# Performance work log

Measured on AMD Instinct MI355X. Metric: run time of the kernel, lower is better.

The kernel has to match this reference:

```python
import jax, jax.numpy as jnp
import numpy as np

LOG_2PI = 1.8378770664093453  # log(2*pi)

B, N_FEAT = 4096, 1024
R, K, D = 64, 32, 16  # n_regions, n_batch (distributions per region), region size


def setup_inputs() -> dict:
    key = jax.random.key(0)
    k1, k2, k3, k4 = jax.random.split(key, 4)
    x = jax.random.normal(k1, (B, N_FEAT), dtype=jnp.float32)
    # Regions: partition-like index sets over the feature space (equal size D).
    regions = jax.random.randint(k2, (R, D), 0, N_FEAT, dtype=jnp.int64)
    # Per-region diag-Gaussian params (means ~ N(0, 0.1), scales near 1.0).
    means = 0.1 * jax.random.normal(k3, (R, K, D), dtype=jnp.float32)
    scales = 0.9 + 0.2 * jax.random.uniform(k4, (R, K, D), dtype=jnp.float32)
    return {"x": x, "regions": regions, "means": means, "scales": scales}


def reference(x, regions, means, scales):
    # Gather per-region features in one shot: [B, R, D]
    xg = x[:, regions]
    # Diag-Gaussian log-prob, broadcast over the K distributions per region.
    # z: [B, R, K, D]
    z = (xg[:, :, None, :] - means[None]) / scales[None]
    log_det = jnp.sum(jnp.log(scales), axis=-1)  # [R, K]
    ll = -0.5 * jnp.sum(z * z, axis=-1) - log_det[None] - 0.5 * D * LOG_2PI
    return ll  # [B, R, K] == stack over regions of MVNDiag.log_prob
```

## Files before the change

kernel.cpp:

```cpp
#include <hip/hip_runtime.h>

#define NB 4096
#define NF 1024
#define NR 64
#define NK 32
#define ND 16
#define BT 8
#define RT 32
#define HALF_D_LOG2PI 14.702988531274762f

__global__ __launch_bounds__(256) void prep_kernel(
    const float* __restrict__ means, const float* __restrict__ scales,
    float* __restrict__ isv, float* __restrict__ nmv, float* __restrict__ cv)
{
    int p = blockIdx.x * 256 + threadIdx.x;
    if (p >= NR * NK) return;
    const float4* m4 = (const float4*)(means + p * ND);
    const float4* s4 = (const float4*)(scales + p * ND);
    float4* i4 = (float4*)(isv + p * ND);
    float4* n4 = (float4*)(nmv + p * ND);
    float ld = 0.f;
#pragma unroll
    for (int q = 0; q < 4; ++q) {
        float4 m = m4[q], s = s4[q];
        float4 iv, nv;
        iv.x = 1.f / s.x; iv.y = 1.f / s.y; iv.z = 1.f / s.z; iv.w = 1.f / s.w;
        nv.x = -m.x * iv.x; nv.y = -m.y * iv.y; nv.z = -m.z * iv.z; nv.w = -m.w * iv.w;
        ld += logf(s.x) + logf(s.y) + logf(s.z) + logf(s.w);
        i4[q] = iv; n4[q] = nv;
    }
    cv[p] = -ld - HALF_D_LOG2PI;
}

__global__ __launch_bounds__(256) void GaussianLayer_64003602645438_kernel(
    const float* __restrict__ x,
    const int* __restrict__ regions,
    const float* __restrict__ isv,
    const float* __restrict__ nmv,
    const float* __restrict__ cv,
    float* __restrict__ out)
{
    __shared__ float xs[BT][NF];
    __shared__ float xg[BT][RT][ND];
    __shared__ int   ridx[RT * ND];

    const int t  = threadIdx.x;
    const int b0 = blockIdx.x * BT;
    const int r0 = blockIdx.y * RT;

    for (int j = t; j < RT * ND; j += 256)
        ridx[j] = regions[r0 * ND + j];

    {
        const float4* xsrc = (const float4*)(x + (size_t)b0 * NF);
        float4* xdst = (float4*)(&xs[0][0]);
#pragma unroll
        for (int j = t; j < BT * NF / 4; j += 256)
            xdst[j] = xsrc[j];
    }
    __syncthreads();

    for (int j = t; j < BT * RT * ND; j += 256) {
        int d  = j & (ND - 1);
        int rl = (j >> 4) & (RT - 1);
        int b  = j >> 9;
        xg[b][rl][d] = xs[b][ridx[rl * ND + d]];
    }
    __syncthreads();

    const int k   = t & 31;
    const int rl8 = t >> 5;

#pragma unroll
    for (int it = 0; it < RT / 8; ++it) {
        const int rl = it * 8 + rl8;
        const int r  = r0 + rl;
        const int pk = r * NK + k;
        const float4* i4 = (const float4*)(isv + pk * ND);
        const float4* n4 = (const float4*)(nmv + pk * ND);
        float4 is0 = i4[0], is1 = i4[1], is2 = i4[2], is3 = i4[3];
        float4 nm0 = n4[0], nm1 = n4[1], nm2 = n4[2], nm3 = n4[3];
        const float c = cv[pk];

#pragma unroll
        for (int b = 0; b < BT; ++b) {
            const float4* xq = (const float4*)(&xg[b][rl][0]);
            float4 x0 = xq[0], x1 = xq[1], x2 = xq[2], x3 = xq[3];
            float acc = 0.f;
#define STEP(xx, ii, nn) { float z = fmaf(xx, ii, nn); acc = fmaf(z, z, acc); }
            STEP(x0.x, is0.x, nm0.x); STEP(x0.y, is0.y, nm0.y);
            STEP(x0.z, is0.z, nm0.z); STEP(x0.w, is0.w, nm0.w);
            STEP(x1.x, is1.x, nm1.x); STEP(x1.y, is1.y, nm1.y);
            STEP(x1.z, is1.z, nm1.z); STEP(x1.w, is1.w, nm1.w);
            STEP(x2.x, is2.x, nm2.x); STEP(x2.y, is2.y, nm2.y);
            STEP(x2.z, is2.z, nm2.z); STEP(x2.w, is2.w, nm2.w);
            STEP(x3.x, is3.x, nm3.x); STEP(x3.y, is3.y, nm3.y);
            STEP(x3.z, is3.z, nm3.z); STEP(x3.w, is3.w, nm3.w);
#undef STEP
            out[(size_t)(b0 + b) * (NR * NK) + r * NK + k] = fmaf(acc, -0.5f, c);
        }
    }
}

extern "C" void kernel_launch(void* const* d_in, const int* in_sizes, int n_in,
                              void* d_out, int out_size, void* d_ws, size_t ws_size,
                              hipStream_t stream) {
    const float* x       = (const float*)d_in[0];
    const int*   regions = (const int*)d_in[1];
    const float* means   = (const float*)d_in[2];
    const float* scales  = (const float*)d_in[3];
    float* out = (float*)d_out;

    float* w   = (float*)d_ws;
    float* isv = w;
    float* nmv = w + NR * NK * ND;
    float* cv  = w + 2 * NR * NK * ND;

    prep_kernel<<<dim3((NR * NK + 255) / 256), 256, 0, stream>>>(means, scales, isv, nmv, cv);

    dim3 grid(NB / BT, NR / RT);
    GaussianLayer_64003602645438_kernel<<<grid, 256, 0, stream>>>(x, regions, isv, nmv, cv, out);
}
```

Before: 95.27 us.

## Recast Gaussian log-prob as bf16 split-precision MFMA GEMM with separate gather pass

Expands the quadratic form into x^2*A + x*B + c and evaluates it per region as a small matrix multiply on MFMA bf16 instructions. x and x^2 are each split into hi/lo bf16 parts to keep precision. A separate gather kernel writes packed bf16 fragments to workspace, and the GEMM kernel reads them with pre-swizzled weight fragments. The extra intermediate round trip (about 16MB written and read back) plus a third launch is traded against the removed scalar FMA work. Weights are plain bf16, which may cost accuracy.

```diff
diff --git a/kernel.cpp b/kernel.cpp
--- a/kernel.cpp
+++ b/kernel.cpp
@@ -1,103 +1,161 @@
 #include <hip/hip_runtime.h>
+#include <hip/hip_bf16.h>
+
+typedef __attribute__((ext_vector_type(8))) short short8;
+typedef __attribute__((ext_vector_type(4))) float floatx4;
 
 #define NB 4096
 #define NF 1024
 #define NR 64
 #define NK 32
 #define ND 16
-#define BT 8
-#define RT 32
 #define HALF_D_LOG2PI 14.702988531274762f
+
+__device__ __forceinline__ unsigned f2bf_bits(float f) {
+    unsigned u = __float_as_uint(f);
+    return (u + 0x7fffu + ((u >> 16) & 1u)) >> 16;
+}
+__device__ __forceinline__ float bf_bits2f(unsigned b) {
+    return __uint_as_float(b << 16);
+}
 
 __global__ __launch_bounds__(256) void prep_kernel(
     const float* __restrict__ means, const float* __restrict__ scales,
-    float* __restrict__ isv, float* __restrict__ nmv, float* __restrict__ cv)
+    unsigned short* __restrict__ wfrag, float* __restrict__ cv)
 {
     int p = blockIdx.x * 256 + threadIdx.x;
     if (p >= NR * NK) return;
-    const float4* m4 = (const float4*)(means + p * ND);
-    const float4* s4 = (const float4*)(scales + p * ND);
-    float4* i4 = (float4*)(isv + p * ND);
-    float4* n4 = (float4*)(nmv + p * ND);
-    float ld = 0.f;
+    int n  = p & 15;
+    int nt = (p >> 4) & 1;
+    int r  = p >> 5;
+
+    const float* m = means  + (size_t)p * ND;
+    const float* s = scales + (size_t)p * ND;
+    float Av[ND], Bv[ND];
+    float csum = 0.f;
 #pragma unroll
-    for (int q = 0; q < 4; ++q) {
-        float4 m = m4[q], s = s4[q];
-        float4 iv, nv;
-        iv.x = 1.f / s.x; iv.y = 1.f / s.y; iv.z = 1.f / s.z; iv.w = 1.f / s.w;
-        nv.x = -m.x * iv.x; nv.y = -m.y * iv.y; nv.z = -m.z * iv.z; nv.w = -m.w * iv.w;
-        ld += logf(s.x) + logf(s.y) + logf(s.z) + logf(s.w);
-        i4[q] = iv; n4[q] = nv;
+    for (int d = 0; d < ND; ++d) {
+        float sd = s[d], md = m[d];
+        float a  = 1.0f / sd;
+        float a2 = a * a;
+        Av[d] = -0.5f * a2;
+        Bv[d] = md * a2;
+        float c = md * a;
+        csum += -0.5f * c * c - logf(sd);
     }
-    cv[p] = -ld - HALF_D_LOG2PI;
+    cv[p] = csum - HALF_D_LOG2PI;
+
+#pragma unroll
+    for (int slot = 0; slot < 4; ++slot) {
+        int ks = slot >> 1;
+#pragma unroll
+        for (int d = 0; d < ND; ++d) {
+            int Kin  = (slot & 1) * 16 + d;
+            int quad = Kin >> 3;
+            int j    = Kin & 7;
+            int lane = quad * 16 + n;
+            size_t idx = ((((size_t)r * 2 + ks) * 2 + nt) * 64 + lane) * 8 + j;
+            float v = (slot < 2) ? Av[d] : Bv[d];
+            wfrag[idx] = (unsigned short)f2bf_bits(v);
+        }
+    }
 }
 
-__global__ __launch_bounds__(256) void GaussianLayer_64003602645438_kernel(
-    const float* __restrict__ x,
-    const int* __restrict__ regions,
-    const float* __restrict__ isv,
-    const float* __restrict__ nmv,
+__global__ __launch_bounds__(256) void gather_kernel(
+    const float* __restrict__ x, const int* __restrict__ regions,
+    unsigned short* __restrict__ xg)
+{
+    __shared__ float xs[8][NF];
+    __shared__ int   ridx[NR * ND];
+
+    const int t  = threadIdx.x;
+    const int b0 = blockIdx.x * 8;
+
+    for (int j = t; j < NR * ND; j += 256) ridx[j] = regions[j];
+    {
+        const float4* src = (const float4*)(x + (size_t)b0 * NF);
+        float4* dst = (float4*)(&xs[0][0]);
+#pragma unroll
+        for (int j = t; j < 8 * NF / 4; j += 256) dst[j] = src[j];
+    }
+    __syncthreads();
+
+#pragma unroll
+    for (int pi = 0; pi < 2; ++pi) {
+        int p  = t + pi * 256;
+        int r  = p & 63;
+        int bl = p >> 6;
+        int b  = b0 + bl;
+        size_t row = ((size_t)(b >> 4) * NR + r) * 16 + (b & 15);
+
+        unsigned pk[32];
+#pragma unroll
+        for (int d = 0; d < ND; d += 2) {
+            float xv0 = xs[bl][ridx[r * ND + d]];
+            float xv1 = xs[bl][ridx[r * ND + d + 1]];
+            float q0 = xv0 * xv0, q1 = xv1 * xv1;
+            unsigned x2h0 = f2bf_bits(q0), x2h1 = f2bf_bits(q1);
+            unsigned x2l0 = f2bf_bits(q0 - bf_bits2f(x2h0));
+            unsigned x2l1 = f2bf_bits(q1 - bf_bits2f(x2h1));
+            unsigned xh0  = f2bf_bits(xv0), xh1 = f2bf_bits(xv1);
+            unsigned xl0  = f2bf_bits(xv0 - bf_bits2f(xh0));
+            unsigned xl1  = f2bf_bits(xv1 - bf_bits2f(xh1));
+            int di = d >> 1;
+            pk[0 * 8 + di] = x2h0 | (x2h1 << 16);
+            pk[1 * 8 + di] = x2l0 | (x2l1 << 16);
+            pk[2 * 8 + di] = xh0  | (xh1  << 16);
+            pk[3 * 8 + di] = xl0  | (xl1  << 16);
+        }
+        uint4* gdst = (uint4*)(xg + row * 64);
+#pragma unroll
+        for (int q = 0; q < 8; ++q) gdst[q] = ((uint4*)pk)[q];
+    }
+}
+
+__global__ __launch_bounds__(256) void gemm_kernel(
+    const unsigned short* __restrict__ xg,
+    const unsigned short* __restrict__ wfrag,
     const float* __restrict__ cv,
     float* __restrict__ out)
 {
-    __shared__ float xs[BT][NF];
-    __shared__ float xg[BT][RT][ND];
-    __shared__ int   ridx[RT * ND];
+    const int t    = threadIdx.x;
+    const int w    = t >> 6;
+    const int L    = t & 63;
+    const int m    = L & 15;
+    const int quad = L >> 4;
+    const int bt16 = blockIdx.x * 4 + w;
+    const int r0   = blockIdx.y * 8;
 
-    const int t  = threadIdx.x;
-    const int b0 = blockIdx.x * BT;
-    const int r0 = blockIdx.y * RT;
+    const short* xgs = (const short*)xg;
+    const short* wfs = (const short*)wfrag;
 
-    for (int j = t; j < RT * ND; j += 256)
-        ridx[j] = regions[r0 * ND + j];
+#pragma unroll 2
+    for (int i = 0; i < 8; ++i) {
+        int r = r0 + i;
+        size_t arow = (((size_t)bt16 * NR + r) * 16 + m) * 64 + quad * 8;
+        short8 a0 = *(const short8*)(xgs + arow);
+        short8 a1 = *(const short8*)(xgs + arow + 32);
+        size_t wb = ((size_t)r * 4) * 512 + L * 8;
+        short8 w00 = *(const short8*)(wfs + wb);
+        short8 w01 = *(const short8*)(wfs + wb + 512);
+        short8 w10 = *(const short8*)(wfs + wb + 1024);
+        short8 w11 = *(const short8*)(wfs + wb + 1536);
 
-    {
-        const float4* xsrc = (const float4*)(x + (size_t)b0 * NF);
-        float4* xdst = (float4*)(&xs[0][0]);
+        floatx4 acc0 = {0.f, 0.f, 0.f, 0.f};
+        floatx4 acc1 = {0.f, 0.f, 0.f, 0.f};
+        acc0 = __builtin_amdgcn_mfma_f32_16x16x32_bf16(a0, w00, acc0, 0, 0, 0);
+        acc0 = __builtin_amdgcn_mfma_f32_16x16x32_bf16(a1, w10, acc0, 0, 0, 0);
+        acc1 = __builtin_amdgcn_mfma_f32_16x16x32_bf16(a0, w01, acc1, 0, 0, 0);
+        acc1 = __builtin_amdgcn_mfma_f32_16x16x32_bf16(a1, w11, acc1, 0, 0, 0);
+
+        float c0 = cv[r * NK + m];
+        float c1 = cv[r * NK + 16 + m];
+        int brow = bt16 * 16 + quad * 4;
 #pragma unroll
-        for (int j = t; j < BT * NF / 4; j += 256)
-            xdst[j] = xsrc[j];
-    }
-    __syncthreads();
-
-    for (int j = t; j < BT * RT * ND; j += 256) {
-        int d  = j & (ND - 1);
-        int rl = (j >> 4) & (RT - 1);
-        int b  = j >> 9;
-        xg[b][rl][d] = xs[b][ridx[rl * ND + d]];
-    }
-    __syncthreads();
-
-    const int k   = t & 31;
-    const int rl8 = t >> 5;
-
-#pragma unroll
-    for (int it = 0; it < RT / 8; ++it) {
-        const int rl = it * 8 + rl8;
-        const int r  = r0 + rl;
-        const int pk = r * NK + k;
-        const float4* i4 = (const float4*)(isv + pk * ND);
-        const float4* n4 = (const float4*)(nmv + pk * ND);
-        float4 is0 = i4[0], is1 = i4[1], is2 = i4[2], is3 = i4[3];
-        float4 nm0 = n4[0], nm1 = n4[1], nm2 = n4[2], nm3 = n4[3];
-        const float c = cv[pk];
-
-#pragma unroll
-        for (int b = 0; b < BT; ++b) {
-            const float4* xq = (const float4*)(&xg[b][rl][0]);
-            float4 x0 = xq[0], x1 = xq[1], x2 = xq[2], x3 = xq[3];
-            float acc = 0.f;
-#define STEP(xx, ii, nn) { float z = fmaf(xx, ii, nn); acc = fmaf(z, z, acc); }
-            STEP(x0.x, is0.x, nm0.x); STEP(x0.y, is0.y, nm0.y);
-            STEP(x0.z, is0.z, nm0.z); STEP(x0.w, is0.w, nm0.w);
-            STEP(x1.x, is1.x, nm1.x); STEP(x1.y, is1.y, nm1.y);
-            STEP(x1.z, is1.z, nm1.z); STEP(x1.w, is1.w, nm1.w);
-            STEP(x2.x, is2.x, nm2.x); STEP(x2.y, is2.y, nm2.y);
-            STEP(x2.z, is2.z, nm2.z); STEP(x2.w, is2.w, nm2.w);
-            STEP(x3.x, is3.x, nm3.x); STEP(x3.y, is3.y, nm3.y);
-            STEP(x3.z, is3.z, nm3.z); STEP(x3.w, is3.w, nm3.w);
-#undef STEP
-            out[(size_t)(b0 + b) * (NR * NK) + r * NK + k] = fmaf(acc, -0.5f, c);
+        for (int g = 0; g < 4; ++g) {
+            size_t ob = (size_t)(brow + g) * (NR * NK) + (size_t)r * NK;
+            out[ob + m]      = acc0[g] + c0;
+            out[ob + 16 + m] = acc1[g] + c1;
         }
     }
 }
@@ -111,13 +169,12 @@
     const float* scales  = (const float*)d_in[3];
     float* out = (float*)d_out;
 
-    float* w   = (float*)d_ws;
-    float* isv = w;
-    float* nmv = w + NR * NK * ND;
-    float* cv  = w + 2 * NR * NK * ND;
+    char* ws = (char*)d_ws;
+    unsigned short* wfrag = (unsigned short*)ws;
+    float*          cvp   = (float*)(ws + 262144);
+    unsigned short* xgp   = (unsigned short*)(ws + 262144 + 8192);
 
-    prep_kernel<<<dim3((NR * NK + 255) / 256), 256, 0, stream>>>(means, scales, isv, nmv, cv);
-
-    dim3 grid(NB / BT, NR / RT);
-    GaussianLayer_64003602645438_kernel<<<grid, 256, 0, stream>>>(x, regions, isv, nmv, cv, out);
+    prep_kernel<<<dim3((NR * NK + 255) / 256), 256, 0, stream>>>(means, scales, wfrag, cvp);
+    gather_kernel<<<dim3(NB / 8), 256, 0, stream>>>(x, regions, xgp);
+    gemm_kernel<<<dim3(NB / 64, 8), 256, 0, stream>>>(xgp, wfrag, cvp, out);
 }
```

After: 107.6 us. +12.9%, slower.
